# Optimization experiments

Hardware: AMD Instinct MI355X
Metric: run time of the kernel (lower is better)

## Reference

```python
import jax, jax.numpy as jnp
import numpy as np

B, N, M, D, H, DK = 4, 2048, 1024, 512, 8, 64  # H*DK == D (required by residual E + E_)
SCALE = 1.0 / np.sqrt(DK)
NEG = -9e15


def setup_inputs() -> dict:
    key = jax.random.key(0)
    ks = jax.random.split(key, 24)
    def W(k, din, dout):
        return (0.02 * jax.random.truncated_normal(k, -2.0, 2.0, (din, dout))).astype(jnp.float32)
    inp = {
        'X': jax.random.normal(ks[0], (B, N, D), jnp.float32),
        'incidence_matrix': jax.random.randint(ks[1], (B, N, M), 0, 2, jnp.int32),
        'attn_bias': jnp.zeros((1,), jnp.float32),
        'E': jax.random.normal(ks[2], (B, M, D), jnp.float32),
        'Wqn': W(ks[3], D, H * DK), 'bqn': jnp.zeros((H * DK,), jnp.float32),
        'Wkn': W(ks[4], D, H * DK), 'bkn': jnp.zeros((H * DK,), jnp.float32),
        'Wvn': W(ks[5], D, H * DK), 'bvn': jnp.zeros((H * DK,), jnp.float32),
        'Wqe': W(ks[6], D, H * DK), 'bqe': jnp.zeros((H * DK,), jnp.float32),
        'Wke': W(ks[7], D, H * DK), 'bke': jnp.zeros((H * DK,), jnp.float32),
        'Wve': W(ks[8], D, H * DK), 'bve': jnp.zeros((H * DK,), jnp.float32),
        'Wm1': W(ks[9], D, D), 'bm1': jnp.zeros((D,), jnp.float32),
        'Wm2': W(ks[10], D, D), 'bm2': jnp.zeros((D,), jnp.float32),
        'g_ln': jnp.ones((D,), jnp.float32), 'b_ln': jnp.zeros((D,), jnp.float32),
    }
    return inp


def _heads(x, Wt, b):
    # [B, L, D] -> [B, H, L, DK]
    b_, l_ = x.shape[0], x.shape[1]
    return (x @ Wt + b).reshape(b_, l_, H, DK).transpose(0, 2, 1, 3)


def _merge(x):
    # [B, H, L, DK] -> [B, L, H*DK]
    b_, _, l_, _ = x.shape
    return x.transpose(0, 2, 1, 3).reshape(b_, l_, H * DK)


def _layernorm(x, g, b, eps=1e-7):
    mu = jnp.mean(x, axis=-1, keepdims=True)
    var = jnp.var(x, axis=-1, keepdims=True)
    return (x - mu) * jax.lax.rsqrt(var + eps) * g + b


def _gelu(x):
    return jax.nn.gelu(x, approximate=False)


def reference(X, incidence_matrix, attn_bias, E,
              Wqn, bqn, Wkn, bkn, Wvn, bvn,
              Wqe, bqe, Wke, bke, Wve, bve,
              Wm1, bm1, Wm2, bm2, g_ln, b_ln):
    q_n = _heads(X, Wqn, bqn)   # [B,H,N,DK]
    k_n = _heads(X, Wkn, bkn)
    v_n = _heads(X, Wvn, bvn)
    q_e = _heads(E, Wqe, bqe)   # [B,H,M,DK]

    # edge attends over nodes: [B,H,M,N], masked by incidence^T
    att_e = jnp.einsum('bhmd,bhnd->bhmn', q_e, k_n) * SCALE
    mask_e = (incidence_matrix > 0).transpose(0, 2, 1)[:, None, :, :]  # [B,1,M,N]
    att_e = jnp.where(mask_e, att_e, NEG)
    w_e = jax.nn.softmax(att_e, axis=-1)
    E_ = _gelu(jnp.einsum('bhmn,bhnd->bhmd', w_e, v_n))
    E_ = _merge(E_)                                   # [B,M,D]
    E_ = _layernorm(E + E_, g_ln, b_ln)
    E_ = _gelu(E_ @ Wm1 + bm1) @ Wm2 + bm2            # MLP

    k_e = _heads(E_, Wke, bke)  # [B,H,M,DK]
    v_e = _heads(E_, Wve, bve)

    # node attends over edges: [B,H,N,M], masked by incidence
    att_n = jnp.einsum('bhnd,bhmd->bhnm', q_n, k_e) * SCALE
    mask_n = (incidence_matrix > 0)[:, None, :, :]    # [B,1,N,M]
    att_n = jnp.where(mask_n, att_n, NEG)
    w_n = jax.nn.softmax(att_n, axis=-1)
    X_ = _gelu(jnp.einsum('bhnm,bhmd->bhnd', w_n, v_e))
    X_ = _merge(X_)                                   # [B,N,D]
    return (X_, E_)
```

## Files before the change

kernel.cpp:

```cpp
#include <hip/hip_runtime.h>

typedef unsigned short u16;
typedef unsigned int   u32;
typedef unsigned long long u64;

typedef __attribute__((ext_vector_type(8))) short  bf16x8;
typedef __attribute__((ext_vector_type(16))) float f32x16;

#define SC2 0.1803368801111243f
#define CS2 11.541560327111707f

__device__ __forceinline__ float bf2f(u16 h) { return __uint_as_float(((u32)h) << 16); }
__device__ __forceinline__ u16 f2bf(float f) {
  u32 u = __float_as_uint(f);
  return (u16)((u + 0x7FFFu + ((u >> 16) & 1u)) >> 16);
}
__device__ __forceinline__ float gelu_f(float x) {
  return 0.5f * x * (1.0f + erff(x * 0.70710678118654752440f));
}
__device__ __forceinline__ void unpack8(uint4 u, float* d) {
  d[0] = __uint_as_float(u.x << 16); d[1] = __uint_as_float(u.x & 0xffff0000u);
  d[2] = __uint_as_float(u.y << 16); d[3] = __uint_as_float(u.y & 0xffff0000u);
  d[4] = __uint_as_float(u.z << 16); d[5] = __uint_as_float(u.z & 0xffff0000u);
  d[6] = __uint_as_float(u.w << 16); d[7] = __uint_as_float(u.w & 0xffff0000u);
}
__device__ __forceinline__ void dma16(const u16* g, u16* l) {
  __builtin_amdgcn_global_load_lds(
      (const __attribute__((address_space(1))) u32*)g,
      (__attribute__((address_space(3))) u32*)l, 16, 0, 0);
}

__global__ void detect_dtype(const u16* __restrict__ X, u32* __restrict__ flag) {
  int lane = threadIdx.x;
  int bad = 0;
  #pragma unroll
  for (int i = 0; i < 8; ++i) {
    u16 v = X[i * 64 + lane];
    int e = (v >> 7) & 0xFF;
    if (e >= 0x88) bad++;
  }
  #pragma unroll
  for (int o = 1; o < 64; o <<= 1) bad += __shfl_xor(bad, o);
  if (lane == 0) *flag = (bad > 16) ? 1u : 0u;
}

__global__ __launch_bounds__(256) void fill_diag(u32* __restrict__ out, float base,
                                                 const u32* __restrict__ flag) {
  float v = base + (*flag ? 4000.0f : 0.0f);
  u16 h = f2bf(v);
  out[blockIdx.x * 256 + threadIdx.x] = (u32)h | ((u32)h << 16);
}

__global__ __launch_bounds__(256) void conv_bf16(const void* __restrict__ src,
                                                 u16* __restrict__ dst, int n,
                                                 const u32* __restrict__ flag) {
  int i = (blockIdx.x * 256 + threadIdx.x) * 8;
  if (i >= n) return;
  if (*flag) {
    const float* s = (const float*)src + i;
    float4 a = *(const float4*)s;
    float4 b = *(const float4*)(s + 4);
    uint4 o;
    o.x = (u32)f2bf(a.x) | ((u32)f2bf(a.y) << 16);
    o.y = (u32)f2bf(a.z) | ((u32)f2bf(a.w) << 16);
    o.z = (u32)f2bf(b.x) | ((u32)f2bf(b.y) << 16);
    o.w = (u32)f2bf(b.z) | ((u32)f2bf(b.w) << 16);
    *(uint4*)(dst + i) = o;
  } else {
    *(uint4*)(dst + i) = *(const uint4*)((const u16*)src + i);
  }
}

__global__ __launch_bounds__(256) void conv_vec10(
    const void* p0, const void* p1, const void* p2, const void* p3, const void* p4,
    const void* p5, const void* p6, const void* p7, const void* p8, const void* p9,
    u16* __restrict__ dst, const u32* __restrict__ flag) {
  const void* ps[10] = {p0, p1, p2, p3, p4, p5, p6, p7, p8, p9};
  int fl = (int)(*flag);
  for (int idx = threadIdx.x; idx < 5120; idx += 256) {
    int slot = idx >> 9, off = idx & 511;
    u16 v;
    if (fl) v = f2bf(((const float*)ps[slot])[off]);
    else    v = ((const u16*)ps[slot])[off];
    dst[idx] = v;
  }
}

__global__ __launch_bounds__(256) void wtrans(
    const void* w0, const void* w1, const void* w2, const void* w3,
    const void* w4, const void* w5, const void* w6, const void* w7,
    u16* __restrict__ WT, const u32* __restrict__ flag) {
  const void* wsrc[8] = {w0, w1, w2, w3, w4, w5, w6, w7};
  __shared__ u16 tile[32][33];
  int z = blockIdx.z;
  const void* W = wsrc[z];
  u16* Wt = WT + (size_t)z * 262144;
  int fl = (int)(*flag);
  int tx = threadIdx.x & 31, ty = threadIdx.x >> 5;
  int bx = blockIdx.x * 32, by = blockIdx.y * 32;
  #pragma unroll
  for (int i = 0; i < 4; ++i) {
    int r = ty + 8 * i;
    size_t src = (size_t)(by + r) * 512 + bx + tx;
    tile[r][tx] = fl ? f2bf(((const float*)W)[src]) : ((const u16*)W)[src];
  }
  __syncthreads();
  #pragma unroll
  for (int i = 0; i < 4; ++i) {
    int r = ty + 8 * i;
    Wt[(size_t)(bx + r) * 512 + by + tx] = tile[tx][r];
  }
}

__global__ __launch_bounds__(256) void emit_out(const u16* __restrict__ src,
                                                void* __restrict__ dst, size_t elem_off,
                                                int n, const u32* __restrict__ flag) {
  int i = (blockIdx.x * 256 + threadIdx.x) * 8;
  if (i >= n) return;
  uint4 u = *(const uint4*)(src + i);
  if (*flag) {
    float d[8]; unpack8(u, d);
    float* o = (float*)dst + elem_off + i;
    *(float4*)o       = *(float4*)&d[0];
    *(float4*)(o + 4) = *(float4*)&d[4];
  } else {
    *(uint4*)((u16*)dst + elem_off + i) = u;
  }
}

__global__ __launch_bounds__(256) void transposeV(const u16* __restrict__ Vp,
                                                  u16* __restrict__ VT, int Lk) {
  __shared__ u16 tile[64][72];
  int t = threadIdx.x;
  int nt = blockIdx.x;
  int bh = blockIdx.y;
  int nw = Lk >> 6;
  const u16* src = Vp + ((size_t)bh * Lk + nt * 64) * 64;
  int key = t >> 2, seg = t & 3;
  int dc0 = seg * 2, dc1 = seg * 2 + 1;
  uint4 a  = *(const uint4*)(src + key * 64 + ((dc0 ^ (key & 7)) << 3));
  uint4 b2 = *(const uint4*)(src + key * 64 + ((dc1 ^ (key & 7)) << 3));
  *(uint4*)&tile[key][dc0 * 8] = a;
  *(uint4*)&tile[key][dc1 * 8] = b2;
  __syncthreads();
  int d = t >> 2;
  u32 wb[8];
  #pragma unroll
  for (int i = 0; i < 8; ++i) {
    u32 lo = tile[seg * 16 + 2 * i][d];
    u32 hi = tile[seg * 16 + 2 * i + 1][d];
    wb[i] = lo | (hi << 16);
  }
  u16* base = VT + (((size_t)bh * nw + nt) * 64 + d) * 64;
  int kc0 = seg * 2, kc1 = seg * 2 + 1;
  uint4 o0; o0.x = wb[0]; o0.y = wb[1]; o0.z = wb[2]; o0.w = wb[3];
  uint4 o1; o1.x = wb[4]; o1.y = wb[5]; o1.z = wb[6]; o1.w = wb[7];
  *(uint4*)(base + ((kc0 ^ (d & 7)) << 3)) = o0;
  *(uint4*)(base + ((kc1 ^ (d & 7)) << 3)) = o1;
}

__global__ __launch_bounds__(256) void pack_rows(const int* __restrict__ inc,
                                                 u64* __restrict__ packNT) {
  int gid  = blockIdx.x * 4 + (threadIdx.x >> 6);
  int lane = threadIdx.x & 63;
  int w  = gid & 15;
  int bn = gid >> 4;
  int b = bn >> 11, n = bn & 2047;
  int v = inc[(size_t)bn * 1024 + (w << 6) + lane];
  u64 mask = __ballot(v > 0);
  if (lane == 0) packNT[((size_t)(b * 16 + w)) * 2048 + n] = mask;
}

__global__ __launch_bounds__(256) void pack_cols(const int* __restrict__ inc,
                                                 u64* __restrict__ packTT) {
  int m = blockIdx.x * 256 + threadIdx.x;
  int w = blockIdx.y;
  int b = blockIdx.z;
  const int* base = inc + ((size_t)b * 2048 + (size_t)w * 64) * 1024 + m;
  u64 out = 0;
  #pragma unroll 8
  for (int j = 0; j < 64; ++j)
    if (base[(size_t)j * 1024] > 0) out |= (1ull << j);
  packTT[((size_t)(b * 32 + w)) * 1024 + m] = out;
}

__global__ __launch_bounds__(256) void gemm_tiled(const u16* __restrict__ A,
                                                  const u16* __restrict__ Wt0, u32 wtStride,
                                                  const u16* __restrict__ bias0, u32 bStride,
                                                  u16* __restrict__ C0, u32 cStride,
                                                  int Mrows, int act, int blocksPerMat,
                                                  int mode, int lkshift) {
  __shared__ u16 As[2][8192];
  __shared__ u16 Bs[2][8192];
  (void)Mrows;
  int mat = blockIdx.x / blocksPerMat;
  int blk = blockIdx.x % blocksPerMat;
  const u16* Wt = Wt0 + (size_t)mat * wtStride;
  const u16* bias = bias0 + (size_t)mat * bStride;
  u16* C = C0 + (size_t)mat * cStride;
  int tm = blk >> 2, tn = blk & 3;
  int m0 = tm * 128, n0 = tn * 128;

  int t = threadIdx.x;
  int wave = t >> 6, lane = t & 63;
  int nl = lane & 31, h32 = lane >> 5;
  int wm = wave >> 1, wn = wave & 1;

  int srow = lane >> 3;
  int gch  = (lane & 7) ^ srow;
  const u16* Ab = A  + ((size_t)m0 + wave * 32) * 512 + (size_t)srow * 512 + gch * 8;
  const u16* Bb = Wt + ((size_t)n0 + wave * 32) * 512 + (size_t)srow * 512 + gch * 8;
  u16* AsW = &As[0][0] + wave * 32 * 64;
  u16* BsW = &Bs[0][0] + wave * 32 * 64;

  #pragma unroll
  for (int c = 0; c < 4; ++c) {
    dma16(Ab + (size_t)c * 8 * 512, AsW + c * 8 * 64);
    dma16(Bb + (size_t)c * 8 * 512, BsW + c * 8 * 64);
  }
  __syncthreads();

  f32x16 a00 = {}, a01 = {}, a10 = {}, a11 = {};

  for (int kk = 0; kk < 8; ++kk) {
    int buf = kk & 1;
    if (kk + 1 < 8) {
      int k0n = (kk + 1) * 64;
      u16* AD = &As[buf ^ 1][0] + wave * 32 * 64;
      u16* BD = &Bs[buf ^ 1][0] + wave * 32 * 64;
      #pragma unroll
      for (int c = 0; c < 4; ++c) {
        dma16(Ab + (size_t)c * 8 * 512 + k0n, AD + c * 8 * 64);
        dma16(Bb + (size_t)c * 8 * 512 + k0n, BD + c * 8 * 64);
      }
    }
    const u16* Ab_s = &As[buf][0];
    const u16* Bb_s = &Bs[buf][0];
    int ar0 = wm * 64 + nl, ar1 = wm * 64 + 32 + nl;
    int br0 = wn * 64 + nl, br1 = wn * 64 + 32 + nl;
    #pragma unroll
    for (int ks = 0; ks < 4; ++ks) {
      int sw = (((ks * 2 + h32) ^ (nl & 7)) << 3);
      bf16x8 fa0 = *(const bf16x8*)(Ab_s + ar0 * 64 + sw);
      bf16x8 fa1 = *(const bf16x8*)(Ab_s + ar1 * 64 + sw);
      bf16x8 fb0 = *(const bf16x8*)(Bb_s + br0 * 64 + sw);
      bf16x8 fb1 = *(const bf16x8*)(Bb_s + br1 * 64 + sw);
      a00 = __builtin_amdgcn_mfma_f32_32x32x16_bf16(fa0, fb0, a00, 0, 0, 0);
      a01 = __builtin_amdgcn_mfma_f32_32x32x16_bf16(fa0, fb1, a01, 0, 0, 0);
      a10 = __builtin_amdgcn_mfma_f32_32x32x16_bf16(fa1, fb0, a10, 0, 0, 0);
      a11 = __builtin_amdgcn_mfma_f32_32x32x16_bf16(fa1, fb1, a11, 0, 0, 0);
    }
    __syncthreads();
  }

  int nw = 1 << (lkshift - 6);
  #pragma unroll
  for (int am = 0; am < 2; ++am) {
    #pragma unroll
    for (int bn = 0; bn < 2; ++bn) {
      const f32x16* accp = am == 0 ? (bn == 0 ? &a00 : &a01)
                                   : (bn == 0 ? &a10 : &a11);
      f32x16 acc = *accp;
      int cn = n0 + wn * 64 + bn * 32 + nl;
      float bv = bf2f(bias[cn]);
      #pragma unroll
      for (int g = 0; g < 16; ++g) {
        int rm = m0 + wm * 64 + am * 32 + (g & 3) + 8 * (g >> 2) + 4 * h32;
        float v = acc[g] + bv;
        if (act) v = gelu_f(v);
        if (mode) {
          int bb = rm >> lkshift;
          int key = rm & ((1 << lkshift) - 1);
          int nt = key >> 6, kl = key & 63;
          int d = cn & 63;
          size_t ad = ((((size_t)bb * 8 + (cn >> 6)) * nw + nt) * 64 + kl) * 64
                      + (((d >> 3) ^ (kl & 7)) << 3) + (d & 7);
          C[ad] = f2bf(v);
        } else {
          C[(size_t)rm * 512 + cn] = f2bf(v);
        }
      }
    }
  }
}

__global__ __launch_bounds__(128, 2) void flash_mfma(
    const u16* __restrict__ Q,
    const u16* __restrict__ Kp,
    const u16* __restrict__ VTp,
    const u64* __restrict__ maskT,
    void* __restrict__ Outv,
    u16* __restrict__ Opart, float* __restrict__ Lpart,
    int Lq, int Lk, int splits, int is_final, const u32* __restrict__ flag) {
  __shared__ u16 K_s[2][4096];
  __shared__ u16 V_s[2][4096];
  __shared__ u16 P_s[2][2048];

  int t = threadIdx.x;
  int wave = t >> 6, lane = t & 63;
  int nl = lane & 31, h32 = lane >> 5;
  int qtiles = Lq >> 6;
  int nwords = Lk >> 6;
  int r2 = blockIdx.x % (qtiles * 32);
  int split = blockIdx.x / (qtiles * 32);
  int qt = r2 % qtiles;
  int bh = r2 / qtiles;
  int h = bh & 7, b = bh >> 3;
  int row0 = qt * 64 + wave * 32;
  int per = nwords / splits;
  int tile0 = split * per;
  int f32o = is_final ? (int)(*flag) : 0;

  bf16x8 qf[4];
  {
    const u16* qp = Q + ((size_t)(b * Lq) + row0 + nl) * 512 + h * 64 + h32 * 8;
    #pragma unroll
    for (int ks = 0; ks < 4; ++ks) qf[ks] = *(const bf16x8*)(qp + ks * 16);
  }
  const u16* Kbh = Kp + (size_t)bh * Lk * 64;
  const u16* Vbh = VTp + (size_t)bh * nwords * 4096;
  const u64* mrow = maskT + (size_t)b * nwords * Lq + row0 + nl;

  f32x16 o0 = {}, o1 = {};
  float lsum = 0.f;

  {
    const u16* TK = Kbh + (size_t)tile0 * 4096;
    const u16* TV = Vbh + (size_t)tile0 * 4096;
    #pragma unroll
    for (int c = 0; c < 4; ++c) {
      int ch = c * 2 + wave;
      dma16(TK + ch * 512 + lane * 8, &K_s[0][ch * 512]);
      dma16(TV + ch * 512 + lane * 8, &V_s[0][ch * 512]);
    }
  }
  __syncthreads();

  for (int i = 0; i < per; ++i) {
    int nt = tile0 + i;
    int buf = i & 1;
    if (i + 1 < per) {
      const u16* TK = Kbh + (size_t)(nt + 1) * 4096;
      const u16* TV = Vbh + (size_t)(nt + 1) * 4096;
      u16* KD = K_s[buf ^ 1];
      u16* VD = V_s[buf ^ 1];
      #pragma unroll
      for (int c = 0; c < 4; ++c) {
        int ch = c * 2 + wave;
        dma16(TK + ch * 512 + lane * 8, KD + ch * 512);
        dma16(TV + ch * 512 + lane * 8, VD + ch * 512);
      }
    }
    u64 mymask = mrow[(size_t)nt * Lq];

    f32x16 s0 = {}, s1 = {};
    #pragma unroll
    for (int ks = 0; ks < 4; ++ks) {
      int ch = ks * 2 + h32;
      bf16x8 k0 = *(const bf16x8*)&K_s[buf][nl * 64 + ((ch ^ (nl & 7)) << 3)];
      bf16x8 k1 = *(const bf16x8*)&K_s[buf][(32 + nl) * 64 + ((ch ^ (nl & 7)) << 3)];
      s0 = __builtin_amdgcn_mfma_f32_32x32x16_bf16(k0, qf[ks], s0, 0, 0, 0);
      s1 = __builtin_amdgcn_mfma_f32_32x32x16_bf16(k1, qf[ks], s1, 0, 0, 0);
    }
    #pragma unroll
    for (int gg = 0; gg < 4; ++gg) {
      u16 w0[4], w1[4];
      #pragma unroll
      for (int r = 0; r < 4; ++r) {
        int g = gg * 4 + r;
        int key = r + 8 * gg + 4 * h32;
        float p0 = ((mymask >> key) & 1ull)
                     ? exp2f(fmaf(s0[g], SC2, -CS2)) : 0.f;
        float p1 = ((mymask >> (key + 32)) & 1ull)
                     ? exp2f(fmaf(s1[g], SC2, -CS2)) : 0.f;
        lsum += p0 + p1;
        w0[r] = f2bf(p0); w1[r] = f2bf(p1);
      }
      uint2 a0, a1;
      a0.x = (u32)w0[0] | ((u32)w0[1] << 16);
      a0.y = (u32)w0[2] | ((u32)w0[3] << 16);
      a1.x = (u32)w1[0] | ((u32)w1[1] << 16);
      a1.y = (u32)w1[2] | ((u32)w1[3] << 16);
      *(uint2*)&P_s[wave][gg * 256 + nl * 8 + 4 * h32]       = a0;
      *(uint2*)&P_s[wave][(4 + gg) * 256 + nl * 8 + 4 * h32] = a1;
    }
    asm volatile("s_waitcnt lgkmcnt(0)" ::: "memory");
    #pragma unroll
    for (int ks2 = 0; ks2 < 4; ++ks2) {
      int ch = ks2 * 2 + h32;
      bf16x8 pf = *(const bf16x8*)&P_s[wave][ch * 256 + nl * 8];
      bf16x8 v0 = *(const bf16x8*)&V_s[buf][nl * 64 + ((ch ^ (nl & 7)) << 3)];
      bf16x8 v1 = *(const bf16x8*)&V_s[buf][(32 + nl) * 64 + ((ch ^ (nl & 7)) << 3)];
      o0 = __builtin_amdgcn_mfma_f32_32x32x16_bf16(pf, v0, o0, 0, 0, 0);
      o1 = __builtin_amdgcn_mfma_f32_32x32x16_bf16(pf, v1, o1, 0, 0, 0);
    }
    __syncthreads();
  }
  lsum += __shfl_xor(lsum, 32);

  if (Opart) {
    u16* ob = Opart + (size_t)split * 2097152;
    #pragma unroll
    for (int g = 0; g < 16; ++g) {
      int m = (g & 3) + 8 * (g >> 2) + 4 * h32;
      size_t base = ((size_t)(b * Lq) + row0 + m) * 512 + h * 64;
      ob[base + nl]      = f2bf(o0[g]);
      ob[base + 32 + nl] = f2bf(o1[g]);
    }
    if (h32 == 0)
      Lpart[(size_t)split * 32768 + ((size_t)(b * Lq) + row0 + nl) * 8 + h] = lsum;
  } else {
    #pragma unroll
    for (int g = 0; g < 16; ++g) {
      int m = (g & 3) + 8 * (g >> 2) + 4 * h32;
      float lv = __shfl(lsum, m);
      float inv = 1.0f / (lv + 1e-30f);
      size_t base = ((size_t)(b * Lq) + row0 + m) * 512 + h * 64;
      float v0 = gelu_f(o0[g] * inv);
      float v1 = gelu_f(o1[g] * inv);
      if (f32o) {
        ((float*)Outv)[base + nl]      = v0;
        ((float*)Outv)[base + 32 + nl] = v1;
      } else {
        ((u16*)Outv)[base + nl]      = f2bf(v0);
        ((u16*)Outv)[base + 32 + nl] = f2bf(v1);
      }
    }
  }
}

__global__ __launch_bounds__(256) void combine_edge(const u16* __restrict__ Op,
                                                    const float* __restrict__ Lp,
                                                    u16* __restrict__ EATT) {
  int r = blockIdx.x;
  int t = threadIdx.x;
  int e = t * 2;
  int h = e >> 6;
  float lv = Lp[r * 8 + h] + Lp[32768 + r * 8 + h] + 1e-30f;
  float inv = 1.0f / lv;
  size_t idx = (size_t)r * 512 + e;
  u32 u0 = *(const u32*)&Op[idx];
  u32 u1 = *(const u32*)&Op[2097152 + idx];
  float a  = bf2f((u16)(u0 & 0xffff)) + bf2f((u16)(u1 & 0xffff));
  float b2 = bf2f((u16)(u0 >> 16))    + bf2f((u16)(u1 >> 16));
  u32 o = (u32)f2bf(gelu_f(a * inv)) | ((u32)f2bf(gelu_f(b2 * inv)) << 16);
  *(u32*)&EATT[idx] = o;
}

__global__ __launch_bounds__(256) void ln_kernel(const u16* __restrict__ E,
                                                 const u16* __restrict__ Ea,
                                                 const u16* __restrict__ g,
                                                 const u16* __restrict__ bb,
                                                 u16* __restrict__ out) {
  int row = blockIdx.x;
  int t = threadIdx.x;
  size_t base = (size_t)row * 512 + t * 2;
  u32 ue = *(const u32*)(E + base);
  u32 ua = *(const u32*)(Ea + base);
  float x0 = bf2f((u16)(ue & 0xffffu)) + bf2f((u16)(ua & 0xffffu));
  float x1 = bf2f((u16)(ue >> 16)) + bf2f((u16)(ua >> 16));
  float s = x0 + x1, q = x0 * x0 + x1 * x1;
  #pragma unroll
  for (int o = 32; o; o >>= 1) { s += __shfl_down(s, o); q += __shfl_down(q, o); }
  __shared__ float red[8];
  int wv = t >> 6, ln = t & 63;
  if (ln == 0) { red[wv] = s; red[4 + wv] = q; }
  __syncthreads();
  s = red[0] + red[1] + red[2] + red[3];
  q = red[4] + red[5] + red[6] + red[7];
  float mean = s * (1.f / 512.f);
  float var  = q * (1.f / 512.f) - mean * mean;
  float rs = rsqrtf(var + 1e-7f);
  u32 ug = *(const u32*)(g + t * 2);
  u32 ub = *(const u32*)(bb + t * 2);
  float y0 = (x0 - mean) * rs * bf2f((u16)(ug & 0xffffu)) + bf2f((u16)(ub & 0xffffu));
  float y1 = (x1 - mean) * rs * bf2f((u16)(ug >> 16)) + bf2f((u16)(ub >> 16));
  *(u32*)(out + base) = (u32)f2bf(y0) | ((u32)f2bf(y1) << 16);
}

extern "C" void kernel_launch(void* const* d_in, const int* in_sizes, int n_in,
                              void* d_out, int out_size, void* d_ws, size_t ws_size,
                              hipStream_t stream) {
  (void)in_sizes; (void)n_in; (void)out_size;
  const int* inc = (const int*)d_in[1];

  char* ws = (char*)d_ws;
  u32* FLAG = (u32*)ws;
  u16* VEC  = (u16*)(ws + 1024);
  u16* WT   = (u16*)(ws + 65536);
  u16* XB   = (u16*)(ws + 8454144);
  u16* EB   = (u16*)(ws + 16842752);
  u16* QN   = (u16*)(ws + 21037056);
  u16* KN   = (u16*)(ws + 29425664);
  u16* VN   = (u16*)(ws + 37814272);
  u16* QE   = (u16*)(ws + 46202880);
  u16* EATT = (u16*)(ws + 50397184);
  u16* EFIN = (u16*)(ws + 54591488);
  u64* PACKT = (u64*)(ws + 58785792);
  u64* PACKN = (u64*)(ws + 59834368);
  const size_t NEEDED = 60882944;
  u16* ELN = (u16*)(ws + 29425664);
  u16* H1  = (u16*)(ws + 33619968);
  u16* KE  = (u16*)(ws + 37814272);
  u16* VE  = (u16*)(ws + 42008576);
  u16* Opart = XB;
  float* Lpart = (float*)(ws + 37814272);
  u16* VTn = (u16*)d_out;
  u16* VTe = EATT;

  detect_dtype<<<1, 64, 0, stream>>>((const u16*)d_in[0], FLAG);

  if (ws_size < NEEDED) {
    fill_diag<<<8192, 256, 0, stream>>>((u32*)d_out,
                                        1000.0f + (float)(ws_size >> 20), FLAG);
    return;
  }

  conv_bf16<<<2048, 256, 0, stream>>>(d_in[0], XB, 4194304, FLAG);
  conv_bf16<<<1024, 256, 0, stream>>>(d_in[3], EB, 2097152, FLAG);
  conv_vec10<<<1, 256, 0, stream>>>(d_in[5], d_in[7], d_in[9], d_in[11], d_in[13],
                                    d_in[15], d_in[17], d_in[19], d_in[20], d_in[21],
                                    VEC, FLAG);
  wtrans<<<dim3(16, 16, 8), 256, 0, stream>>>(d_in[4], d_in[6], d_in[8], d_in[10],
                                              d_in[12], d_in[14], d_in[16], d_in[18],
                                              WT, FLAG);
  pack_cols<<<dim3(4, 32, 4), 256, 0, stream>>>(inc, PACKT);
  pack_rows<<<32768, 256, 0, stream>>>(inc, PACKN);

  gemm_tiled<<<256, 256, 0, stream>>>(XB, WT, 0, VEC, 0,
                                      QN, 0, 8192, 0, 256, 0, 11);
  gemm_tiled<<<512, 256, 0, stream>>>(XB, WT + 262144, 262144, VEC + 512, 512,
                                      KN, 4194304, 8192, 0, 256, 1, 11);
  gemm_tiled<<<128, 256, 0, stream>>>(EB, WT + 3 * 262144, 0, VEC + 3 * 512, 0,
                                      QE, 0, 4096, 0, 128, 0, 11);

  transposeV<<<dim3(32, 32), 256, 0, stream>>>(VN, VTn, 2048);

  flash_mfma<<<1024, 128, 0, stream>>>(QE, KN, VTn, PACKT, nullptr,
                                       Opart, Lpart, 1024, 2048, 2, 0, FLAG);
  combine_edge<<<4096, 256, 0, stream>>>(Opart, Lpart, EATT);

  ln_kernel<<<4096, 256, 0, stream>>>(EB, EATT, VEC + 8 * 512, VEC + 9 * 512, ELN);
  gemm_tiled<<<128, 256, 0, stream>>>(ELN, WT + 6 * 262144, 0, VEC + 6 * 512, 0,
                                      H1, 0, 4096, 1, 128, 0, 11);
  gemm_tiled<<<128, 256, 0, stream>>>(H1, WT + 7 * 262144, 0, VEC + 7 * 512, 0,
                                      EFIN, 0, 4096, 0, 128, 0, 11);
  emit_out<<<1024, 256, 0, stream>>>(EFIN, d_out, 4194304, 2097152, FLAG);

  gemm_tiled<<<256, 256, 0, stream>>>(EFIN, WT + 4 * 262144, 262144, VEC + 4 * 512, 512,
                                      KE, 2097152, 4096, 0, 128, 1, 10);
  transposeV<<<dim3(16, 32), 256, 0, stream>>>(VE, VTe, 1024);

  flash_mfma<<<1024, 128, 0, stream>>>(QN, KE, VTe, PACKN, d_out,
                                       nullptr, nullptr, 2048, 1024, 1, 1, FLAG);
}
```

Baseline: 398.1 us.

## Fuse combine into layernorm, merge QKV GEMMs, write output from GEMM epilogue

Merges the combine_edge and ln_kernel passes into a single ln_fused kernel that reads the split-K partials directly. The QN/KN/VN projections now run as one launch, with a per-matrix mode bitmask choosing the swizzled layout. The final MLP GEMM writes the f32/bf16 output directly, which removes the emit_out pass. In flash, the masking is rewritten to compute exp unconditionally and pack bf16 by truncation instead of rounding. These changes cut launches and intermediate memory traffic, at the cost of slightly different rounding of P and extra stores in the GEMM epilogue.

Result: no change. 391.2 us (-1.7%).

```diff
diff --git a/kernel.cpp b/kernel.cpp
--- a/kernel.cpp
+++ b/kernel.cpp
@@ -112,22 +112,6 @@
   }
 }
 
-__global__ __launch_bounds__(256) void emit_out(const u16* __restrict__ src,
-                                                void* __restrict__ dst, size_t elem_off,
-                                                int n, const u32* __restrict__ flag) {
-  int i = (blockIdx.x * 256 + threadIdx.x) * 8;
-  if (i >= n) return;
-  uint4 u = *(const uint4*)(src + i);
-  if (*flag) {
-    float d[8]; unpack8(u, d);
-    float* o = (float*)dst + elem_off + i;
-    *(float4*)o       = *(float4*)&d[0];
-    *(float4*)(o + 4) = *(float4*)&d[4];
-  } else {
-    *(uint4*)((u16*)dst + elem_off + i) = u;
-  }
-}
-
 __global__ __launch_bounds__(256) void transposeV(const u16* __restrict__ Vp,
                                                   u16* __restrict__ VT, int Lk) {
   __shared__ u16 tile[64][72];
@@ -188,16 +172,19 @@
                                                   const u16* __restrict__ Wt0, u32 wtStride,
                                                   const u16* __restrict__ bias0, u32 bStride,
                                                   u16* __restrict__ C0, u32 cStride,
-                                                  int Mrows, int act, int blocksPerMat,
-                                                  int mode, int lkshift) {
+                                                  int act, int blocksPerMat,
+                                                  u32 modeMask, int lkshift,
+                                                  void* __restrict__ out2, size_t out2_off,
+                                                  const u32* __restrict__ flag) {
   __shared__ u16 As[2][8192];
   __shared__ u16 Bs[2][8192];
-  (void)Mrows;
   int mat = blockIdx.x / blocksPerMat;
   int blk = blockIdx.x % blocksPerMat;
   const u16* Wt = Wt0 + (size_t)mat * wtStride;
   const u16* bias = bias0 + (size_t)mat * bStride;
   u16* C = C0 + (size_t)mat * cStride;
+  int mode = (modeMask >> mat) & 1u;
+  int f32o = out2 ? (int)(*flag) : 0;
   int tm = blk >> 2, tn = blk & 3;
   int m0 = tm * 128, n0 = tn * 128;
 
@@ -277,7 +264,12 @@
                       + (((d >> 3) ^ (kl & 7)) << 3) + (d & 7);
           C[ad] = f2bf(v);
         } else {
-          C[(size_t)rm * 512 + cn] = f2bf(v);
+          size_t ad = (size_t)rm * 512 + cn;
+          C[ad] = f2bf(v);
+          if (out2) {
+            if (f32o) ((float*)out2)[out2_off + ad] = v;
+            else      ((u16*)out2)[out2_off + ad] = f2bf(v);
+          }
         }
       }
     }
@@ -352,6 +344,8 @@
       }
     }
     u64 mymask = mrow[(size_t)nt * Lq];
+    u32 mlo = (u32)mymask;
+    u32 mhi = (u32)(mymask >> 32);
 
     f32x16 s0 = {}, s1 = {};
     #pragma unroll
@@ -364,23 +358,22 @@
     }
     #pragma unroll
     for (int gg = 0; gg < 4; ++gg) {
-      u16 w0[4], w1[4];
+      float pv0[4], pv1[4];
       #pragma unroll
       for (int r = 0; r < 4; ++r) {
         int g = gg * 4 + r;
         int key = r + 8 * gg + 4 * h32;
-        float p0 = ((mymask >> key) & 1ull)
-                     ? exp2f(fmaf(s0[g], SC2, -CS2)) : 0.f;
-        float p1 = ((mymask >> (key + 32)) & 1ull)
-                     ? exp2f(fmaf(s1[g], SC2, -CS2)) : 0.f;
-        lsum += p0 + p1;
-        w0[r] = f2bf(p0); w1[r] = f2bf(p1);
+        float e0 = exp2f(fmaf(s0[g], SC2, -CS2));
+        float e1 = exp2f(fmaf(s1[g], SC2, -CS2));
+        pv0[r] = ((mlo >> key) & 1u) ? e0 : 0.f;
+        pv1[r] = ((mhi >> key) & 1u) ? e1 : 0.f;
+        lsum += pv0[r] + pv1[r];
       }
       uint2 a0, a1;
-      a0.x = (u32)w0[0] | ((u32)w0[1] << 16);
-      a0.y = (u32)w0[2] | ((u32)w0[3] << 16);
-      a1.x = (u32)w1[0] | ((u32)w1[1] << 16);
-      a1.y = (u32)w1[2] | ((u32)w1[3] << 16);
+      a0.x = (__float_as_uint(pv0[0]) >> 16) | (__float_as_uint(pv0[1]) & 0xffff0000u);
+      a0.y = (__float_as_uint(pv0[2]) >> 16) | (__float_as_uint(pv0[3]) & 0xffff0000u);
+      a1.x = (__float_as_uint(pv1[0]) >> 16) | (__float_as_uint(pv1[1]) & 0xffff0000u);
+      a1.y = (__float_as_uint(pv1[2]) >> 16) | (__float_as_uint(pv1[3]) & 0xffff0000u);
       *(uint2*)&P_s[wave][gg * 256 + nl * 8 + 4 * h32]       = a0;
       *(uint2*)&P_s[wave][(4 + gg) * 256 + nl * 8 + 4 * h32] = a1;
     }
@@ -429,9 +422,12 @@
   }
 }
 
-__global__ __launch_bounds__(256) void combine_edge(const u16* __restrict__ Op,
-                                                    const float* __restrict__ Lp,
-                                                    u16* __restrict__ EATT) {
+__global__ __launch_bounds__(256) void ln_fused(const u16* __restrict__ Op,
+                                                const float* __restrict__ Lp,
+                                                const u16* __restrict__ E,
+                                                const u16* __restrict__ g,
+                                                const u16* __restrict__ bb,
+                                                u16* __restrict__ out) {
   int r = blockIdx.x;
   int t = threadIdx.x;
   int e = t * 2;
@@ -441,24 +437,11 @@
   size_t idx = (size_t)r * 512 + e;
   u32 u0 = *(const u32*)&Op[idx];
   u32 u1 = *(const u32*)&Op[2097152 + idx];
-  float a  = bf2f((u16)(u0 & 0xffff)) + bf2f((u16)(u1 & 0xffff));
-  float b2 = bf2f((u16)(u0 >> 16))    + bf2f((u16)(u1 >> 16));
-  u32 o = (u32)f2bf(gelu_f(a * inv)) | ((u32)f2bf(gelu_f(b2 * inv)) << 16);
-  *(u32*)&EATT[idx] = o;
-}
-
-__global__ __launch_bounds__(256) void ln_kernel(const u16* __restrict__ E,
-                                                 const u16* __restrict__ Ea,
-                                                 const u16* __restrict__ g,
-                                                 const u16* __restrict__ bb,
-                                                 u16* __restrict__ out) {
-  int row = blockIdx.x;
-  int t = threadIdx.x;
-  size_t base = (size_t)row * 512 + t * 2;
-  u32 ue = *(const u32*)(E + base);
-  u32 ua = *(const u32*)(Ea + base);
-  float x0 = bf2f((u16)(ue & 0xffffu)) + bf2f((u16)(ua & 0xffffu));
-  float x1 = bf2f((u16)(ue >> 16)) + bf2f((u16)(ua >> 16));
+  u32 ue = *(const u32*)&E[idx];
+  float x0 = bf2f((u16)(ue & 0xffffu)) +
+             gelu_f((bf2f((u16)(u0 & 0xffffu)) + bf2f((u16)(u1 & 0xffffu))) * inv);
+  float x1 = bf2f((u16)(ue >> 16)) +
+             gelu_f((bf2f((u16)(u0 >> 16)) + bf2f((u16)(u1 >> 16))) * inv);
   float s = x0 + x1, q = x0 * x0 + x1 * x1;
   #pragma unroll
   for (int o = 32; o; o >>= 1) { s += __shfl_down(s, o); q += __shfl_down(q, o); }
@@ -471,11 +454,11 @@
   float mean = s * (1.f / 512.f);
   float var  = q * (1.f / 512.f) - mean * mean;
   float rs = rsqrtf(var + 1e-7f);
-  u32 ug = *(const u32*)(g + t * 2);
-  u32 ub = *(const u32*)(bb + t * 2);
+  u32 ug = *(const u32*)(g + e);
+  u32 ub = *(const u32*)(bb + e);
   float y0 = (x0 - mean) * rs * bf2f((u16)(ug & 0xffffu)) + bf2f((u16)(ub & 0xffffu));
   float y1 = (x1 - mean) * rs * bf2f((u16)(ug >> 16)) + bf2f((u16)(ub >> 16));
-  *(u32*)(out + base) = (u32)f2bf(y0) | ((u32)f2bf(y1) << 16);
+  *(u32*)(out + idx) = (u32)f2bf(y0) | ((u32)f2bf(y1) << 16);
 }
 
 extern "C" void kernel_launch(void* const* d_in, const int* in_sizes, int n_in,
@@ -502,11 +485,11 @@
   u16* ELN = (u16*)(ws + 29425664);
   u16* H1  = (u16*)(ws + 33619968);
   u16* KE  = (u16*)(ws + 37814272);
-  u16* VE  = (u16*)(ws + 42008576);
   u16* Opart = XB;
   float* Lpart = (float*)(ws + 37814272);
   u16* VTn = (u16*)d_out;
   u16* VTe = EATT;
+  u16* VE  = (u16*)(ws + 42008576);
 
   detect_dtype<<<1, 64, 0, stream>>>((const u16*)d_in[0], FLAG);
 
@@ -527,28 +510,28 @@
   pack_cols<<<dim3(4, 32, 4), 256, 0, stream>>>(inc, PACKT);
   pack_rows<<<32768, 256, 0, stream>>>(inc, PACKN);
 
-  gemm_tiled<<<256, 256, 0, stream>>>(XB, WT, 0, VEC, 0,
-                                      QN, 0, 8192, 0, 256, 0, 11);
-  gemm_tiled<<<512, 256, 0, stream>>>(XB, WT + 262144, 262144, VEC + 512, 512,
-                                      KN, 4194304, 8192, 0, 256, 1, 11);
+  gemm_tiled<<<768, 256, 0, stream>>>(XB, WT, 262144, VEC, 512,
+                                      QN, 4194304, 0, 256, 0b110u, 11,
+                                      nullptr, 0, FLAG);
   gemm_tiled<<<128, 256, 0, stream>>>(EB, WT + 3 * 262144, 0, VEC + 3 * 512, 0,
-                                      QE, 0, 4096, 0, 128, 0, 11);
+                                      QE, 0, 0, 128, 0, 11, nullptr, 0, FLAG);
 
   transposeV<<<dim3(32, 32), 256, 0, stream>>>(VN, VTn, 2048);
 
   flash_mfma<<<1024, 128, 0, stream>>>(QE, KN, VTn, PACKT, nullptr,
                                        Opart, Lpart, 1024, 2048, 2, 0, FLAG);
-  combine_edge<<<4096, 256, 0, stream>>>(Opart, Lpart, EATT);
-
-  ln_kernel<<<4096, 256, 0, stream>>>(EB, EATT, VEC + 8 * 512, VEC + 9 * 512, ELN);
+
+  ln_fused<<<4096, 256, 0, stream>>>(Opart, Lpart, EB,
+                                     VEC + 8 * 512, VEC + 9 * 512, ELN);
   gemm_tiled<<<128, 256, 0, stream>>>(ELN, WT + 6 * 262144, 0, VEC + 6 * 512, 0,
-                                      H1, 0, 4096, 1, 128, 0, 11);
+                                      H1, 0, 1, 128, 0, 11, nullptr, 0, FLAG);
   gemm_tiled<<<128, 256, 0, stream>>>(H1, WT + 7 * 262144, 0, VEC + 7 * 512, 0,
-                                      EFIN, 0, 4096, 0, 128, 0, 11);
-  emit_out<<<1024, 256, 0, stream>>>(EFIN, d_out, 4194304, 2097152, FLAG);
+                                      EFIN, 0, 0, 128, 0, 11,
+                                      d_out, 4194304, FLAG);
 
   gemm_tiled<<<256, 256, 0, stream>>>(EFIN, WT + 4 * 262144, 262144, VEC + 4 * 512, 512,
-                                      KE, 2097152, 4096, 0, 128, 1, 10);
+                                      KE, 2097152, 0, 128, 0b11u, 10,
+                                      nullptr, 0, FLAG);
   transposeV<<<dim3(16, 32), 256, 0, stream>>>(VE, VTe, 1024);
 
   flash_mfma<<<1024, 128, 0, stream>>>(QN, KE, VTe, PACKN, d_out,
```
